# Performance work log

Measured on AMD Instinct MI355X. Metric: run time of the kernel, lower is better.

Reference implementation:

```python
import jax, jax.numpy as jnp
import numpy as np

BN_EPS = 1e-5
NN_EPS = 1e-8
K = 3


def conv_bn_relu(x, W, b, gamma, beta, mean, var):
    # x: [B, Cin, N]; W: [Cout, Cin] (1x1 conv); BN in inference mode w/ running stats
    y = jnp.einsum('bcn,oc->bon', x, W) + b[None, :, None]
    y = (y - mean[None, :, None]) * (gamma / jnp.sqrt(var + BN_EPS))[None, :, None] + beta[None, :, None]
    return jax.nn.relu(y)


def three_interpolation(p1, p2, f2):
    # p1: [B, N1, 3] unknown xyz; p2: [B, N2, 3] known xyz; f2: [B, C, N2]
    # squared pairwise distances via the expansion trick (avoids [B,N1,N2,3])
    d2 = (jnp.sum(p1 * p1, -1)[:, :, None]
          + jnp.sum(p2 * p2, -1)[:, None, :]
          - 2.0 * jnp.einsum('bnd,bmd->bnm', p1, p2))  # [B, N1, N2]
    neg_d2, idx = jax.lax.top_k(-d2, K)                 # 3 nearest
    dist = -neg_d2                                      # squared dists, [B, N1, 3]
    recip = 1.0 / (dist + NN_EPS)
    weight = recip / jnp.sum(recip, axis=-1, keepdims=True)  # [B, N1, 3]
    f2t = jnp.transpose(f2, (0, 2, 1))                  # [B, N2, C]
    gathered = jax.vmap(lambda f, i: f[i])(f2t, idx)    # [B, N1, 3, C]
    return jnp.einsum('bnkc,bnk->bcn', gathered, weight)  # [B, C, N1]


def setup_inputs() -> dict:
    key = jax.random.key(0)
    ks = jax.random.split(key, 16)
    B, N1, N2 = 8, 16384, 4096
    mlp = [256, 128, 128]
    inp = {
        'p1': jax.random.normal(ks[0], (B, N1, 3), jnp.float32),
        'p2': jax.random.normal(ks[1], (B, N2, 3), jnp.float32),
        'f2': jax.random.normal(ks[2], (B, mlp[0], N2), jnp.float32),
    }
    kidx = 3
    for li in range(len(mlp) - 1):
        cin, cout = mlp[li], mlp[li + 1]
        inp[f'W{li}'] = jax.random.normal(ks[kidx], (cout, cin), jnp.float32) * (1.0 / np.sqrt(cin)); kidx += 1
        inp[f'b{li}'] = jnp.zeros((cout,), jnp.float32)
        inp[f'gamma{li}'] = jnp.ones((cout,), jnp.float32)
        inp[f'beta{li}'] = jnp.zeros((cout,), jnp.float32)
        inp[f'mean{li}'] = jax.random.normal(ks[kidx], (cout,), jnp.float32) * 0.1; kidx += 1
        inp[f'var{li}'] = jax.random.uniform(ks[kidx], (cout,), jnp.float32, 0.5, 1.5); kidx += 1
    return inp


def reference(p1, p2, f2,
              W0, b0, gamma0, beta0, mean0, var0,
              W1, b1, gamma1, beta1, mean1, var1):
    f = conv_bn_relu(f2, W0, b0, gamma0, beta0, mean0, var0)
    f = conv_bn_relu(f, W1, b1, gamma1, beta1, mean1, var1)
    return three_interpolation(p1, p2, f)
```

## Files before the change

### kernel.cpp

```cpp
#include <hip/hip_runtime.h>

#define B_    8
#define N1_   16384
#define N2_   4096
#define NTOT_ (B_ * N1_)

typedef float v2f __attribute__((ext_vector_type(2)));

__device__ __forceinline__ float np_sumsq(float x, float y, float z)
{
#pragma clang fp contract(off)
    return ((x * x + y * y) + z * z);
}

__global__ __launch_bounds__(256) void fold_kernel(
    const float* __restrict__ W, const float* __restrict__ bias,
    const float* __restrict__ gamma, const float* __restrict__ beta,
    const float* __restrict__ mean, const float* __restrict__ var,
    float* __restrict__ Wp, float* __restrict__ bp, int Cout, int Cin)
{
    int t = blockIdx.x * 256 + threadIdx.x;
    if (t < Cout * Cin) {
        int o = t / Cin;
        float s = gamma[o] / sqrtf(var[o] + 1e-5f);
        Wp[t] = W[t] * s;
    }
    if (t < Cout) {
        float s = gamma[t] / sqrtf(var[t] + 1e-5f);
        bp[t] = beta[t] + (bias[t] - mean[t]) * s;
    }
}

__global__ __launch_bounds__(256) void q4planar_kernel(
    const float* __restrict__ p2, float4* __restrict__ qA,
    float4* __restrict__ qB)
{
    const int t = blockIdx.x * 256 + threadIdx.x;
    const float* a = p2 + 6 * (size_t)t;
    const float x0 = a[0], y0 = a[1], z0 = a[2];
    const float x1 = a[3], y1 = a[4], z1 = a[5];
    qA[t] = make_float4(x0, x1, y0, y1);
    qB[t] = make_float4(z0, z1, np_sumsq(x0, y0, z0), np_sumsq(x1, y1, z1));
}

template <int CIN, bool TRANS>
__global__ __launch_bounds__(256) void gemm_relu_kernel(
    const float* __restrict__ X, const float* __restrict__ Wp,
    const float* __restrict__ bp, float* __restrict__ Y)
{
    __shared__ float A_lds[32][136];
    __shared__ float B_lds[32][128];

    const int b  = blockIdx.y;
    const int n0 = blockIdx.x * 128;
    const int tid = threadIdx.x;
    const int ty = tid >> 4;
    const int tx = tid & 15;
    const float* Xb = X + (size_t)b * CIN * N2_;

    float acc[8][8];
#pragma unroll
    for (int i = 0; i < 8; ++i)
#pragma unroll
        for (int j = 0; j < 8; ++j) acc[i][j] = 0.f;

    const int a_kq = (tid & 7) * 4;
    const int a_r0 = tid >> 3;
    const int b_n4 = (tid & 31) * 4;
    const int b_k0 = tid >> 5;

    for (int k0 = 0; k0 < CIN; k0 += 32) {
#pragma unroll
        for (int i = 0; i < 4; ++i) {
            const int row = a_r0 + 32 * i;
            const float4 v = *(const float4*)&Wp[(size_t)row * CIN + k0 + a_kq];
            A_lds[a_kq + 0][row] = v.x;
            A_lds[a_kq + 1][row] = v.y;
            A_lds[a_kq + 2][row] = v.z;
            A_lds[a_kq + 3][row] = v.w;
        }
#pragma unroll
        for (int i = 0; i < 4; ++i) {
            const int krow = b_k0 + 8 * i;
            *(float4*)&B_lds[krow][b_n4] =
                *(const float4*)&Xb[(size_t)(k0 + krow) * N2_ + n0 + b_n4];
        }
        __syncthreads();

#pragma unroll
        for (int kk = 0; kk < 32; ++kk) {
            const float4 a0 = *(const float4*)&A_lds[kk][ty * 4];
            const float4 a1 = *(const float4*)&A_lds[kk][64 + ty * 4];
            const float4 bq0 = *(const float4*)&B_lds[kk][tx * 4];
            const float4 bq1 = *(const float4*)&B_lds[kk][64 + tx * 4];
            const float av[8] = {a0.x, a0.y, a0.z, a0.w, a1.x, a1.y, a1.z, a1.w};
            const float bv[8] = {bq0.x, bq0.y, bq0.z, bq0.w, bq1.x, bq1.y, bq1.z, bq1.w};
#pragma unroll
            for (int i = 0; i < 8; ++i)
#pragma unroll
                for (int j = 0; j < 8; ++j)
                    acc[i][j] = fmaf(av[i], bv[j], acc[i][j]);
        }
        __syncthreads();
    }

    float bias_v[8];
#pragma unroll
    for (int i = 0; i < 8; ++i) {
        const int r = (i < 4) ? (ty * 4 + i) : (64 + ty * 4 + (i - 4));
        bias_v[i] = bp[r];
    }

    if (!TRANS) {
#pragma unroll
        for (int i = 0; i < 8; ++i) {
            const int r = (i < 4) ? (ty * 4 + i) : (64 + ty * 4 + (i - 4));
            float* yrow = Y + ((size_t)b * 128 + r) * N2_ + n0;
            float4 v0, v1;
            v0.x = fmaxf(acc[i][0] + bias_v[i], 0.f);
            v0.y = fmaxf(acc[i][1] + bias_v[i], 0.f);
            v0.z = fmaxf(acc[i][2] + bias_v[i], 0.f);
            v0.w = fmaxf(acc[i][3] + bias_v[i], 0.f);
            v1.x = fmaxf(acc[i][4] + bias_v[i], 0.f);
            v1.y = fmaxf(acc[i][5] + bias_v[i], 0.f);
            v1.z = fmaxf(acc[i][6] + bias_v[i], 0.f);
            v1.w = fmaxf(acc[i][7] + bias_v[i], 0.f);
            *(float4*)(yrow + tx * 4) = v0;
            *(float4*)(yrow + 64 + tx * 4) = v1;
        }
    } else {
        float (*T)[132] = (float(*)[132])&A_lds[0][0];
#pragma unroll
        for (int s = 0; s < 4; ++s) {
            if ((tx >> 3) == (s & 1)) {
                const int joff = (s >> 1) * 4;
                const int cl0 = (tx & 7) * 4;
#pragma unroll
                for (int i = 0; i < 8; ++i) {
                    const int r = (i < 4) ? (ty * 4 + i) : (64 + ty * 4 + (i - 4));
#pragma unroll
                    for (int j = 0; j < 4; ++j)
                        T[cl0 + j][r] = fmaxf(acc[i][j + joff] + bias_v[i], 0.f);
                }
            }
            __syncthreads();
#pragma unroll
            for (int p = 0; p < 4; ++p) {
                const int row = (tid >> 5) + 8 * p;
                const float4 v = *(const float4*)&T[row][(tid & 31) * 4];
                float* orow = Y + ((size_t)b * N2_ + n0 + 32 * s + row) * 128;
                *(float4*)&orow[(tid & 31) * 4] = v;
            }
            __syncthreads();
        }
    }
}

__device__ __forceinline__ void ins3(const float t, const int jj,
    float& d0, float& d1, float& d2v, int& i0, int& i1, int& i2)
{
    if (t < d2v) {
        const bool c1 = t < d1, c0 = t < d0;
        d2v = c1 ? d1 : t;                 i2 = c1 ? i1 : jj;
        const float nd1 = c1 ? (c0 ? d0 : t) : d1;
        const int   ni1 = c1 ? (c0 ? i0 : jj) : i1;
        d1 = nd1;                          i1 = ni1;
        d0 = c0 ? t : d0;                  i0 = c0 ? jj : i0;
    }
}

__global__ __launch_bounds__(256, 8) void knn_phase1(
    const float* __restrict__ p1, const float4* __restrict__ qA,
    const float4* __restrict__ qB,
    float* __restrict__ part_d, int* __restrict__ part_i)
{
#pragma clang fp contract(off)
    __shared__ float4 sA[512];
    __shared__ float4 sB[512];

    const int tid = threadIdx.x;
    const int chunk = blockIdx.x & 3;
    const int g = (blockIdx.x >> 2) * 256 + tid;
    const int b = g >> 14;

    const float px = p1[3 * (size_t)g + 0];
    const float py = p1[3 * (size_t)g + 1];
    const float pz = p1[3 * (size_t)g + 2];
    const float s1 = np_sumsq(px, py, pz);

    const v2f px2 = {px, px};
    const v2f py2 = {py, py};
    const v2f pz2 = {pz, pz};
    const v2f s12 = {s1, s1};
    const v2f m2  = {-2.0f, -2.0f};

    const float4* gA = qA + (size_t)b * (N2_ / 2) + chunk * 512;
    const float4* gB = qB + (size_t)b * (N2_ / 2) + chunk * 512;
    sA[tid] = gA[tid];  sA[tid + 256] = gA[tid + 256];
    sB[tid] = gB[tid];  sB[tid + 256] = gB[tid + 256];
    __syncthreads();

    float d0 = 1e30f, d1 = 1e30f, d2v = 1e30f;
    int i0 = 0, i1 = 0, i2 = 0;
    const int jbase = chunk * 1024;

    for (int p4 = 0; p4 < 512; p4 += 4) {
        v2f tt[4];
#pragma unroll
        for (int u = 0; u < 4; ++u) {
            const float4 A  = sA[p4 + u];
            const float4 Bq = sB[p4 + u];
            const v2f x01 = {A.x, A.y};
            const v2f y01 = {A.z, A.w};
            const v2f z01 = {Bq.x, Bq.y};
            const v2f w01 = {Bq.z, Bq.w};
            const v2f zz  = z01 * pz2;
            const v2f dot = __builtin_elementwise_fma(px2, x01,
                              __builtin_elementwise_fma(py2, y01, zz));
            const v2f ss  = s12 + w01;
            tt[u] = __builtin_elementwise_fma(m2, dot, ss);
        }
#pragma unroll
        for (int u = 0; u < 4; ++u) {
            const float t0 = tt[u].x, t1 = tt[u].y;
            if (__any(fminf(t0, t1) < d2v)) {
                const int j0 = jbase + 2 * (p4 + u);
                ins3(t0, j0,     d0, d1, d2v, i0, i1, i2);
                ins3(t1, j0 + 1, d0, d1, d2v, i0, i1, i2);
            }
        }
    }

    part_d[(0 * 4 + chunk) * NTOT_ + g] = d0;
    part_d[(1 * 4 + chunk) * NTOT_ + g] = d1;
    part_d[(2 * 4 + chunk) * NTOT_ + g] = d2v;
    part_i[(0 * 4 + chunk) * NTOT_ + g] = i0;
    part_i[(1 * 4 + chunk) * NTOT_ + g] = i1;
    part_i[(2 * 4 + chunk) * NTOT_ + g] = i2;
}

__global__ __launch_bounds__(256) void knn_merge(
    const float* __restrict__ part_d, const int* __restrict__ part_i,
    int* __restrict__ idx_ws, float* __restrict__ w_ws)
{
    const int g = blockIdx.x * 256 + threadIdx.x;

    float d0 = 1e30f, d1 = 1e30f, d2v = 1e30f;
    int i0 = 0, i1 = 0, i2 = 0;

#pragma unroll
    for (int c = 0; c < 4; ++c) {
#pragma unroll
        for (int k = 0; k < 3; ++k) {
            const float t = part_d[(k * 4 + c) * NTOT_ + g];
            const int  jj = part_i[(k * 4 + c) * NTOT_ + g];
            if (t < d2v) {
                const bool c1 = t < d1, c0 = t < d0;
                d2v = c1 ? d1 : t;                 i2 = c1 ? i1 : jj;
                const float nd1 = c1 ? (c0 ? d0 : t) : d1;
                const int   ni1 = c1 ? (c0 ? i0 : jj) : i1;
                d1 = nd1;                          i1 = ni1;
                d0 = c0 ? t : d0;                  i0 = c0 ? jj : i0;
            }
        }
    }

    float w0, w1, w2;
    {
#pragma clang fp contract(off)
        const float r0 = 1.0f / (d0 + 1e-8f);
        const float r1 = 1.0f / (d1 + 1e-8f);
        const float r2 = 1.0f / (d2v + 1e-8f);
        const float rs = (r0 + r1) + r2;
        w0 = r0 / rs;
        w1 = r1 / rs;
        w2 = r2 / rs;
    }

    idx_ws[g]             = i0;
    idx_ws[NTOT_ + g]     = i1;
    idx_ws[2 * NTOT_ + g] = i2;
    w_ws[g]               = w0;
    w_ws[NTOT_ + g]       = w1;
    w_ws[2 * NTOT_ + g]   = w2;
}

__global__ __launch_bounds__(256) void gather_kernel(
    const float* __restrict__ f_t, const int* __restrict__ idx_ws,
    const float* __restrict__ w_ws, float* __restrict__ out)
{
    const int tid = threadIdx.x;
    const int lane = tid & 63, cg = tid >> 6;
    const int g = blockIdx.x * 64 + lane;
    const int b = g >> 14, n = g & 16383;

    const int i0 = idx_ws[g];
    const int i1 = idx_ws[NTOT_ + g];
    const int i2 = idx_ws[2 * NTOT_ + g];
    const float w0 = w_ws[g];
    const float w1 = w_ws[NTOT_ + g];
    const float w2 = w_ws[2 * NTOT_ + g];

    const float* base = f_t + (size_t)b * N2_ * 128 + cg * 32;
    const float4* r0 = (const float4*)(base + (size_t)i0 * 128);
    const float4* r1 = (const float4*)(base + (size_t)i1 * 128);
    const float4* r2 = (const float4*)(base + (size_t)i2 * 128);

    float acc[32];
#pragma unroll
    for (int q = 0; q < 8; ++q) {
        const float4 a = r0[q], bb = r1[q], c = r2[q];
        acc[4 * q + 0] = fmaf(w0, a.x, fmaf(w1, bb.x, w2 * c.x));
        acc[4 * q + 1] = fmaf(w0, a.y, fmaf(w1, bb.y, w2 * c.y));
        acc[4 * q + 2] = fmaf(w0, a.z, fmaf(w1, bb.z, w2 * c.z));
        acc[4 * q + 3] = fmaf(w0, a.w, fmaf(w1, bb.w, w2 * c.w));
    }

    float* ob = out + ((size_t)b * 128 + cg * 32) * N1_ + n;
#pragma unroll
    for (int c = 0; c < 32; ++c)
        __builtin_nontemporal_store(acc[c], ob + (size_t)c * N1_);
}

extern "C" void kernel_launch(void* const* d_in, const int* in_sizes, int n_in,
                              void* d_out, int out_size, void* d_ws, size_t ws_size,
                              hipStream_t stream)
{
    const float* p1  = (const float*)d_in[0];
    const float* p2  = (const float*)d_in[1];
    const float* f2  = (const float*)d_in[2];
    const float* W0  = (const float*)d_in[3];
    const float* b0  = (const float*)d_in[4];
    const float* g0  = (const float*)d_in[5];
    const float* be0 = (const float*)d_in[6];
    const float* m0  = (const float*)d_in[7];
    const float* v0  = (const float*)d_in[8];
    const float* W1  = (const float*)d_in[9];
    const float* b1  = (const float*)d_in[10];
    const float* g1  = (const float*)d_in[11];
    const float* be1 = (const float*)d_in[12];
    const float* m1  = (const float*)d_in[13];
    const float* v1  = (const float*)d_in[14];

    char* ws = (char*)d_ws;
    float4* qA  = (float4*)(ws);
    float4* qB  = (float4*)(ws + (256 << 10));
    float*  W0p = (float*)(ws + (512 << 10));
    float*  b0p = (float*)(ws + (640 << 10));
    float*  W1p = (float*)(ws + (644 << 10));
    float*  b1p = (float*)(ws + (708 << 10));
    float*  h   = (float*)(ws + ((size_t)1 << 20));
    float*  f_t = (float*)(ws + ((size_t)17 << 20));
    int*    idxw= (int*)  (ws + ((size_t)33 << 20));
    float*  wgt = (float*)(ws + ((size_t)35 << 20));
    float*  pd  = (float*)(ws + ((size_t)1 << 20));
    int*    pi  = (int*)  (ws + ((size_t)9 << 20));

    fold_kernel<<<128, 256, 0, stream>>>(W0, b0, g0, be0, m0, v0, W0p, b0p, 128, 256);
    fold_kernel<<<64, 256, 0, stream>>>(W1, b1, g1, be1, m1, v1, W1p, b1p, 128, 128);
    q4planar_kernel<<<(B_ * N2_ / 2) / 256, 256, 0, stream>>>(p2, qA, qB);

    gemm_relu_kernel<256, false><<<dim3(32, 8), 256, 0, stream>>>(f2, W0p, b0p, h);
    gemm_relu_kernel<128, true ><<<dim3(32, 8), 256, 0, stream>>>(h, W1p, b1p, f_t);

    knn_phase1<<<(NTOT_ / 256) * 4, 256, 0, stream>>>(p1, qA, qB, pd, pi);
    knn_merge<<<NTOT_ / 256, 256, 0, stream>>>(pd, pi, idxw, wgt);
    gather_kernel<<<NTOT_ / 64, 256, 0, stream>>>(f_t, idxw, wgt, (float*)d_out);
}
```

Before: 358.6 us.

## Two-pass KNN: branchless min/max top-3 distances, then threshold-filtered index pass

```diff
diff --git a/kernel.cpp b/kernel.cpp
--- a/kernel.cpp
+++ b/kernel.cpp
@@ -11,6 +11,40 @@
 {
 #pragma clang fp contract(off)
     return ((x * x + y * y) + z * z);
+}
+
+__device__ __forceinline__ void ins3(const float t, const int jj,
+    float& d0, float& d1, float& d2v, int& i0, int& i1, int& i2)
+{
+    if (t < d2v) {
+        const bool c1 = t < d1, c0 = t < d0;
+        d2v = c1 ? d1 : t;                 i2 = c1 ? i1 : jj;
+        const float nd1 = c1 ? (c0 ? d0 : t) : d1;
+        const int   ni1 = c1 ? (c0 ? i0 : jj) : i1;
+        d1 = nd1;                          i1 = ni1;
+        d0 = c0 ? t : d0;                  i0 = c0 ? jj : i0;
+    }
+}
+
+__device__ __forceinline__ void dist4(
+    const float4* __restrict__ sA, const float4* __restrict__ sB, int p4,
+    v2f px2, v2f py2, v2f pz2, v2f s12, v2f m2, v2f tt[4])
+{
+#pragma clang fp contract(off)
+#pragma unroll
+    for (int uu = 0; uu < 4; ++uu) {
+        const float4 A  = sA[p4 + uu];
+        const float4 Bq = sB[p4 + uu];
+        const v2f x01 = {A.x, A.y};
+        const v2f y01 = {A.z, A.w};
+        const v2f z01 = {Bq.x, Bq.y};
+        const v2f w01 = {Bq.z, Bq.w};
+        const v2f zz  = z01 * pz2;
+        const v2f dot = __builtin_elementwise_fma(px2, x01,
+                          __builtin_elementwise_fma(py2, y01, zz));
+        const v2f ss  = s12 + w01;
+        tt[uu] = __builtin_elementwise_fma(m2, dot, ss);
+    }
 }
 
 __global__ __launch_bounds__(256) void fold_kernel(
@@ -156,87 +190,83 @@
     }
 }
 
-__device__ __forceinline__ void ins3(const float t, const int jj,
-    float& d0, float& d1, float& d2v, int& i0, int& i1, int& i2)
-{
-    if (t < d2v) {
-        const bool c1 = t < d1, c0 = t < d0;
-        d2v = c1 ? d1 : t;                 i2 = c1 ? i1 : jj;
-        const float nd1 = c1 ? (c0 ? d0 : t) : d1;
-        const int   ni1 = c1 ? (c0 ? i0 : jj) : i1;
-        d1 = nd1;                          i1 = ni1;
-        d0 = c0 ? t : d0;                  i0 = c0 ? jj : i0;
-    }
-}
-
-__global__ __launch_bounds__(256, 8) void knn_phase1(
+__global__ __launch_bounds__(256, 4) void knn_phase1(
     const float* __restrict__ p1, const float4* __restrict__ qA,
     const float4* __restrict__ qB,
     float* __restrict__ part_d, int* __restrict__ part_i)
 {
 #pragma clang fp contract(off)
-    __shared__ float4 sA[512];
-    __shared__ float4 sB[512];
+    __shared__ float4 sA[1024];
+    __shared__ float4 sB[1024];
 
     const int tid = threadIdx.x;
-    const int chunk = blockIdx.x & 3;
-    const int g = (blockIdx.x >> 2) * 256 + tid;
+    const int chunk = blockIdx.x & 1;
+    const int g = (blockIdx.x >> 1) * 256 + tid;
     const int b = g >> 14;
 
     const float px = p1[3 * (size_t)g + 0];
     const float py = p1[3 * (size_t)g + 1];
     const float pz = p1[3 * (size_t)g + 2];
-    const float s1 = np_sumsq(px, py, pz);
+    const float s1q = np_sumsq(px, py, pz);
 
     const v2f px2 = {px, px};
     const v2f py2 = {py, py};
     const v2f pz2 = {pz, pz};
-    const v2f s12 = {s1, s1};
+    const v2f s12 = {s1q, s1q};
     const v2f m2  = {-2.0f, -2.0f};
 
-    const float4* gA = qA + (size_t)b * (N2_ / 2) + chunk * 512;
-    const float4* gB = qB + (size_t)b * (N2_ / 2) + chunk * 512;
-    sA[tid] = gA[tid];  sA[tid + 256] = gA[tid + 256];
-    sB[tid] = gB[tid];  sB[tid + 256] = gB[tid + 256];
+    const float4* gA = qA + (size_t)b * (N2_ / 2) + chunk * 1024;
+    const float4* gB = qB + (size_t)b * (N2_ / 2) + chunk * 1024;
+#pragma unroll
+    for (int i = 0; i < 4; ++i) {
+        sA[tid + i * 256] = gA[tid + i * 256];
+        sB[tid + i * 256] = gB[tid + i * 256];
+    }
     __syncthreads();
 
     float d0 = 1e30f, d1 = 1e30f, d2v = 1e30f;
+    for (int p4 = 0; p4 < 1024; p4 += 4) {
+        v2f tt[4];
+        dist4(sA, sB, p4, px2, py2, pz2, s12, m2, tt);
+#pragma unroll
+        for (int uu = 0; uu < 4; ++uu) {
+            const float t0 = tt[uu].x, t1 = tt[uu].y;
+            const float u  = fminf(t0, t1);
+            const float v  = fmaxf(t0, t1);
+            const float u2 = fmaxf(d0, u);
+            d0 = fminf(d0, u);
+            const float vv = fminf(d1, v);
+            const float ww = fmaxf(d1, v);
+            d1 = fminf(u2, vv);
+            const float x  = fmaxf(u2, vv);
+            d2v = fminf(d2v, fminf(x, ww));
+        }
+    }
+    const float thr = d2v;
+
+    float dd0 = 1e30f, dd1 = 1e30f, dd2 = 1e30f;
     int i0 = 0, i1 = 0, i2 = 0;
-    const int jbase = chunk * 1024;
-
-    for (int p4 = 0; p4 < 512; p4 += 4) {
+    const int jbase = chunk * 2048;
+    for (int p4 = 0; p4 < 1024; p4 += 4) {
         v2f tt[4];
-#pragma unroll
-        for (int u = 0; u < 4; ++u) {
-            const float4 A  = sA[p4 + u];
-            const float4 Bq = sB[p4 + u];
-            const v2f x01 = {A.x, A.y};
-            const v2f y01 = {A.z, A.w};
-            const v2f z01 = {Bq.x, Bq.y};
-            const v2f w01 = {Bq.z, Bq.w};
-            const v2f zz  = z01 * pz2;
-            const v2f dot = __builtin_elementwise_fma(px2, x01,
-                              __builtin_elementwise_fma(py2, y01, zz));
-            const v2f ss  = s12 + w01;
-            tt[u] = __builtin_elementwise_fma(m2, dot, ss);
-        }
-#pragma unroll
-        for (int u = 0; u < 4; ++u) {
-            const float t0 = tt[u].x, t1 = tt[u].y;
-            if (__any(fminf(t0, t1) < d2v)) {
-                const int j0 = jbase + 2 * (p4 + u);
-                ins3(t0, j0,     d0, d1, d2v, i0, i1, i2);
-                ins3(t1, j0 + 1, d0, d1, d2v, i0, i1, i2);
+        dist4(sA, sB, p4, px2, py2, pz2, s12, m2, tt);
+#pragma unroll
+        for (int uu = 0; uu < 4; ++uu) {
+            const float t0 = tt[uu].x, t1 = tt[uu].y;
+            if (__any(fminf(t0, t1) <= thr)) {
+                const int j0 = jbase + 2 * (p4 + uu);
+                ins3(t0, j0,     dd0, dd1, dd2, i0, i1, i2);
+                ins3(t1, j0 + 1, dd0, dd1, dd2, i0, i1, i2);
             }
         }
     }
 
-    part_d[(0 * 4 + chunk) * NTOT_ + g] = d0;
-    part_d[(1 * 4 + chunk) * NTOT_ + g] = d1;
-    part_d[(2 * 4 + chunk) * NTOT_ + g] = d2v;
-    part_i[(0 * 4 + chunk) * NTOT_ + g] = i0;
-    part_i[(1 * 4 + chunk) * NTOT_ + g] = i1;
-    part_i[(2 * 4 + chunk) * NTOT_ + g] = i2;
+    part_d[(0 * 2 + chunk) * NTOT_ + g] = dd0;
+    part_d[(1 * 2 + chunk) * NTOT_ + g] = dd1;
+    part_d[(2 * 2 + chunk) * NTOT_ + g] = dd2;
+    part_i[(0 * 2 + chunk) * NTOT_ + g] = i0;
+    part_i[(1 * 2 + chunk) * NTOT_ + g] = i1;
+    part_i[(2 * 2 + chunk) * NTOT_ + g] = i2;
 }
 
 __global__ __launch_bounds__(256) void knn_merge(
@@ -249,11 +279,11 @@
     int i0 = 0, i1 = 0, i2 = 0;
 
 #pragma unroll
-    for (int c = 0; c < 4; ++c) {
+    for (int c = 0; c < 2; ++c) {
 #pragma unroll
         for (int k = 0; k < 3; ++k) {
-            const float t = part_d[(k * 4 + c) * NTOT_ + g];
-            const int  jj = part_i[(k * 4 + c) * NTOT_ + g];
+            const float t = part_d[(k * 2 + c) * NTOT_ + g];
+            const int  jj = part_i[(k * 2 + c) * NTOT_ + g];
             if (t < d2v) {
                 const bool c1 = t < d1, c0 = t < d0;
                 d2v = c1 ? d1 : t;                 i2 = c1 ? i1 : jj;
@@ -363,7 +393,7 @@
     gemm_relu_kernel<256, false><<<dim3(32, 8), 256, 0, stream>>>(f2, W0p, b0p, h);
     gemm_relu_kernel<128, true ><<<dim3(32, 8), 256, 0, stream>>>(h, W1p, b1p, f_t);
 
-    knn_phase1<<<(NTOT_ / 256) * 4, 256, 0, stream>>>(p1, qA, qB, pd, pi);
+    knn_phase1<<<(NTOT_ / 256) * 2, 256, 0, stream>>>(p1, qA, qB, pd, pi);
     knn_merge<<<NTOT_ / 256, 256, 0, stream>>>(pd, pi, idxw, wgt);
     gather_kernel<<<NTOT_ / 64, 256, 0, stream>>>(f_t, idxw, wgt, (float*)d_out);
 }
```

Result: slower. 454.5 us (+26.7%).
